# Performance work log

Hardware: AMD Instinct MI355X
Metric: run time of the kernel (lower is better)

## Reference

```python
import jax, jax.numpy as jnp
import numpy as np

B, S, D = 4, 4096, 64

def setup_inputs() -> dict:
    key = jax.random.key(0)
    kq, kk, kv = jax.random.split(key, 3)
    q = jax.random.normal(kq, (B, S, D), dtype=jnp.float32)
    k = jax.random.normal(kk, (B, S, D), dtype=jnp.float32)
    v = jax.random.normal(kv, (B, S, D), dtype=jnp.float32)
    return {"q": q, "k": k, "v": v}

def reference(q, k, v):
    d_k = k.shape[-1]
    # scores: [B, S, S]
    scores = jnp.einsum('bqd,bkd->bqk', q, k) / jnp.sqrt(jnp.asarray(d_k, q.dtype))
    s = scores.shape[-1]
    # causal mask: disallow j > i (strict upper triangle)
    causal = jnp.tril(jnp.ones((scores.shape[-2], s), dtype=bool))
    scores = jnp.where(causal, scores, jnp.asarray(-jnp.inf, scores.dtype))
    norm_scores = jax.nn.softmax(scores, axis=-1)
    return jnp.einsum('bqk,bkd->bqd', norm_scores, v)
```

## Files before the change

kernel.cpp:

```cpp
#include <hip/hip_runtime.h>

#define B_ 4
#define S_ 4096
#define D_ 64

typedef __attribute__((ext_vector_type(8))) short short8;
typedef __attribute__((ext_vector_type(4))) float f32x4;
typedef __attribute__((ext_vector_type(16))) float f32x16;
typedef __attribute__((ext_vector_type(4))) int int4v;
typedef __attribute__((ext_vector_type(2))) unsigned uint2v;
typedef unsigned short u16;

__device__ __forceinline__ unsigned pack_bf2(float a, float b) {
  unsigned ua = __float_as_uint(a) + 0x8000u;
  unsigned ub = __float_as_uint(b) + 0x8000u;
  return __builtin_amdgcn_perm(ub, ua, 0x07060302);
}

__device__ __forceinline__ float fexp2(float x) {
#if __has_builtin(__builtin_amdgcn_exp2f)
  return __builtin_amdgcn_exp2f(x);
#else
  return exp2f(x);
#endif
}

__device__ __forceinline__ uint2v permswap(unsigned a, unsigned b) {
#if __has_builtin(__builtin_amdgcn_permlane32_swap)
  return __builtin_amdgcn_permlane32_swap(a, b, false, false);
#else
  int h = (threadIdx.x >> 5) & 1;
  unsigned ta = __shfl_xor(a, 32);
  unsigned tb = __shfl_xor(b, 32);
  uint2v r;
  r[0] = h ? tb : a;
  r[1] = h ? b : ta;
  return r;
#endif
}

__global__ __launch_bounds__(256) void cvt_all_k(const float* __restrict__ q,
                                                 const float* __restrict__ k,
                                                 const float* __restrict__ v,
                                                 u16* __restrict__ wsQ,
                                                 u16* __restrict__ wsK,
                                                 u16* __restrict__ wsV) {
  int blk = blockIdx.x;
  if (blk < 1024) {
    const float* src = (blk < 512) ? q : k;
    u16* dst = (blk < 512) ? wsQ : wsK;
    float scale = (blk < 512) ? 0.18033688011112042f : 1.0f;
    int t = ((blk & 511) << 8) + threadIdx.x;
    const f32x4* s4 = (const f32x4*)src;
    f32x4 a = s4[2 * t], b = s4[2 * t + 1];
    int4v r;
    r[0] = (int)pack_bf2(a[0] * scale, a[1] * scale);
    r[1] = (int)pack_bf2(a[2] * scale, a[3] * scale);
    r[2] = (int)pack_bf2(b[0] * scale, b[1] * scale);
    r[3] = (int)pack_bf2(b[2] * scale, b[3] * scale);
    *(int4v*)(dst + 8 * (long)t) = r;
  } else {
    int t = ((blk - 1024) << 8) + threadIdx.x;
    int lane = t & 63;
    int J  = (t >> 6) & 3;
    int dt = (t >> 8) & 1;
    int ck = (t >> 9) & 63;
    int b  = t >> 15;
    int row = ck * 64 + J * 16 + (lane >> 5) * 8;
    int col = dt * 32 + (lane & 31);
    const float* src = v + ((long)(b * S_ + row)) * D_ + col;
    float e[8];
#pragma unroll
    for (int i = 0; i < 8; i++) e[i] = src[(long)i * D_];
    int4v r;
    r[0] = (int)pack_bf2(e[0], e[1]);
    r[1] = (int)pack_bf2(e[2], e[3]);
    r[2] = (int)pack_bf2(e[4], e[5]);
    r[3] = (int)pack_bf2(e[6], e[7]);
    *(int4v*)(wsV + 8 * (long)t) = r;
  }
}

#define MFMA32(a, bb, cc) __builtin_amdgcn_mfma_f32_32x32x16_bf16((a), (bb), (cc), 0, 0, 0)

__global__ __launch_bounds__(512, 2) void attn_k(const u16* __restrict__ wsQ,
                                                 const u16* __restrict__ wsK,
                                                 const u16* __restrict__ wsV,
                                                 float* __restrict__ out) {
  int bid = blockIdx.x;
  int b   = bid & 3;
  int g   = 63 - (bid >> 2);
  int tid = threadIdx.x;
  int w = tid >> 6, lane = tid & 63, c2 = lane & 31, h = lane >> 5;
  int cmax = g;
  int q0 = g * 64;

  __shared__ float sMem[8][2176];
  __shared__ float sML[8][2][32];

  float* W = &sMem[w][0];

  short8 qf[2][4];
#pragma unroll
  for (int t = 0; t < 2; t++)
#pragma unroll
    for (int kk = 0; kk < 4; kk++)
      qf[t][kk] = *(const short8*)(wsQ + ((long)(b * S_ + q0 + 32 * t + c2)) * D_ +
                                   kk * 16 + h * 8);

  f32x16 o[2][2];
#pragma unroll
  for (int t = 0; t < 2; t++)
#pragma unroll
    for (int dt = 0; dt < 2; dt++)
#pragma unroll
      for (int r = 0; r < 16; r++) o[t][dt][r] = 0.f;
  float lp[2] = {0.f, 0.f};

  const u16* kbase = wsK + ((long)(b * S_ + c2)) * D_ + h * 8;
  const u16* vbase = wsV + ((long)(b * 64)) * 4096 + (long)lane * 8;

  for (int ck = w; ck <= cmax; ck += 8) {
    const u16* kp = kbase + (long)ck * 64 * D_;
    short8 kf[2][4];
#pragma unroll
    for (int jt = 0; jt < 2; jt++)
#pragma unroll
      for (int kk = 0; kk < 4; kk++)
        kf[jt][kk] = *(const short8*)(kp + jt * 32 * D_ + kk * 16);
    const u16* vp = vbase + (long)ck * 4096;
    short8 vf[2][4];
#pragma unroll
    for (int dt = 0; dt < 2; dt++)
#pragma unroll
      for (int J = 0; J < 4; J++)
        vf[dt][J] = *(const short8*)(vp + (dt * 4 + J) * 512);

#pragma unroll
    for (int t = 0; t < 2; t++) {
      f32x16 s[2];
#pragma unroll
      for (int r = 0; r < 16; r++) { s[0][r] = 0.f; s[1][r] = 0.f; }
#pragma unroll
      for (int kk = 0; kk < 4; kk++) {
        s[0] = MFMA32(kf[0][kk], qf[t][kk], s[0]);
        s[1] = MFMA32(kf[1][kk], qf[t][kk], s[1]);
      }

      if (ck == cmax) {
        int dq = 32 * t + c2;
#pragma unroll
        for (int r = 0; r < 16; r++) {
          int row = (r & 3) + 8 * (r >> 2) + 4 * h;
          if (row      > dq) s[0][r] = -1e30f;
          if (row + 32 > dq) s[1][r] = -1e30f;
        }
      }

      float su0 = 0.f, su1 = 0.f, su2 = 0.f, su3 = 0.f;
#pragma unroll
      for (int r = 0; r < 4; r++) {
        s[0][r]      = fexp2(s[0][r]);      su0 += s[0][r];
        s[0][r + 4]  = fexp2(s[0][r + 4]);  su1 += s[0][r + 4];
        s[0][r + 8]  = fexp2(s[0][r + 8]);  su2 += s[0][r + 8];
        s[0][r + 12] = fexp2(s[0][r + 12]); su3 += s[0][r + 12];
        s[1][r]      = fexp2(s[1][r]);      su0 += s[1][r];
        s[1][r + 4]  = fexp2(s[1][r + 4]);  su1 += s[1][r + 4];
        s[1][r + 8]  = fexp2(s[1][r + 8]);  su2 += s[1][r + 8];
        s[1][r + 12] = fexp2(s[1][r + 12]); su3 += s[1][r + 12];
      }
      lp[t] += (su0 + su1) + (su2 + su3);

      short8 p[4];
#pragma unroll
      for (int jt = 0; jt < 2; jt++) {
        unsigned Dw[8];
#pragma unroll
        for (int gg = 0; gg < 4; gg++) {
          Dw[2 * gg]     = pack_bf2(s[jt][4 * gg],     s[jt][4 * gg + 1]);
          Dw[2 * gg + 1] = pack_bf2(s[jt][4 * gg + 2], s[jt][4 * gg + 3]);
        }
#pragma unroll
        for (int e = 0; e < 2; e++) {
          uint2v r0 = permswap(Dw[4 * e],     Dw[4 * e + 2]);
          uint2v r1 = permswap(Dw[4 * e + 1], Dw[4 * e + 3]);
          int4v pw;
          pw[0] = (int)r0[0]; pw[1] = (int)r1[0];
          pw[2] = (int)r0[1]; pw[3] = (int)r1[1];
          p[2 * jt + e] = __builtin_bit_cast(short8, pw);
        }
      }

#pragma unroll
      for (int J = 0; J < 4; J++) {
        o[t][0] = MFMA32(vf[0][J], p[J], o[t][0]);
        o[t][1] = MFMA32(vf[1][J], p[J], o[t][1]);
      }
    }
  }

#pragma unroll
  for (int t = 0; t < 2; t++) {
    float lt = lp[t];
    lt += __shfl_xor(lt, 32);
    if (h == 0) sML[w][t][c2] = lt;
  }

  for (int t = 0; t < 2; t++) {
    __syncthreads();
#pragma unroll
    for (int dt = 0; dt < 2; dt++)
#pragma unroll
      for (int grp = 0; grp < 4; grp++) {
        f32x4 t4;
        t4[0] = o[t][dt][4 * grp];     t4[1] = o[t][dt][4 * grp + 1];
        t4[2] = o[t][dt][4 * grp + 2]; t4[3] = o[t][dt][4 * grp + 3];
        *(f32x4*)&W[c2 * 68 + 32 * dt + 8 * grp + 4 * h] = t4;
      }
    __syncthreads();

    int q = tid >> 4, d4 = tid & 15;
    float L = 0.f;
    f32x4 acc = {0.f, 0.f, 0.f, 0.f};
#pragma unroll
    for (int w2 = 0; w2 < 8; w2++) {
      L += sML[w2][t][q];
      f32x4 pv = *(f32x4*)&sMem[w2][q * 68 + d4 * 4];
#pragma unroll
      for (int i = 0; i < 4; i++) acc[i] += pv[i];
    }
    float inv = 1.f / L;
    f32x4 r;
#pragma unroll
    for (int i = 0; i < 4; i++) r[i] = acc[i] * inv;
    *(f32x4*)(out + ((long)(b * S_ + q0 + 32 * t + q)) * D_ + d4 * 4) = r;
  }
}

extern "C" void kernel_launch(void* const* d_in, const int* in_sizes, int n_in,
                              void* d_out, int out_size, void* d_ws, size_t ws_size,
                              hipStream_t stream) {
  const float* q = (const float*)d_in[0];
  const float* k = (const float*)d_in[1];
  const float* v = (const float*)d_in[2];
  float* out = (float*)d_out;

  u16* wsQ = (u16*)d_ws;
  u16* wsK = wsQ + (long)B_ * S_ * D_;
  u16* wsV = wsK + (long)B_ * S_ * D_;

  cvt_all_k<<<1536, 256, 0, stream>>>(q, k, v, wsQ, wsK, wsV);
  attn_k<<<256, 512, 0, stream>>>(wsQ, wsK, wsV, out);
}
```

Before: 92.17 us.

## Fuse fp32-to-bf16 conversion into attention kernel, drop separate convert pass

Removes the separate conversion kernel that wrote bf16 copies of Q, K and a pre-permuted V to workspace. The attention kernel now reads fp32 Q/K/V directly and converts to bf16 in registers, applying the softmax scale to Q on load. This saves a kernel launch and a full round trip through workspace memory. In exchange, each K/V chunk is reread as fp32 and reconverted by every query block that uses it, which doubles the load bytes and adds ALU work inside the main loop. The V loads are now strided, eight separate 4-byte reads per fragment.

```diff
diff --git a/kernel.cpp b/kernel.cpp
--- a/kernel.cpp
+++ b/kernel.cpp
@@ -39,54 +39,24 @@
 #endif
 }
 
-__global__ __launch_bounds__(256) void cvt_all_k(const float* __restrict__ q,
-                                                 const float* __restrict__ k,
-                                                 const float* __restrict__ v,
-                                                 u16* __restrict__ wsQ,
-                                                 u16* __restrict__ wsK,
-                                                 u16* __restrict__ wsV) {
-  int blk = blockIdx.x;
-  if (blk < 1024) {
-    const float* src = (blk < 512) ? q : k;
-    u16* dst = (blk < 512) ? wsQ : wsK;
-    float scale = (blk < 512) ? 0.18033688011112042f : 1.0f;
-    int t = ((blk & 511) << 8) + threadIdx.x;
-    const f32x4* s4 = (const f32x4*)src;
-    f32x4 a = s4[2 * t], b = s4[2 * t + 1];
-    int4v r;
-    r[0] = (int)pack_bf2(a[0] * scale, a[1] * scale);
-    r[1] = (int)pack_bf2(a[2] * scale, a[3] * scale);
-    r[2] = (int)pack_bf2(b[0] * scale, b[1] * scale);
-    r[3] = (int)pack_bf2(b[2] * scale, b[3] * scale);
-    *(int4v*)(dst + 8 * (long)t) = r;
-  } else {
-    int t = ((blk - 1024) << 8) + threadIdx.x;
-    int lane = t & 63;
-    int J  = (t >> 6) & 3;
-    int dt = (t >> 8) & 1;
-    int ck = (t >> 9) & 63;
-    int b  = t >> 15;
-    int row = ck * 64 + J * 16 + (lane >> 5) * 8;
-    int col = dt * 32 + (lane & 31);
-    const float* src = v + ((long)(b * S_ + row)) * D_ + col;
-    float e[8];
-#pragma unroll
-    for (int i = 0; i < 8; i++) e[i] = src[(long)i * D_];
-    int4v r;
-    r[0] = (int)pack_bf2(e[0], e[1]);
-    r[1] = (int)pack_bf2(e[2], e[3]);
-    r[2] = (int)pack_bf2(e[4], e[5]);
-    r[3] = (int)pack_bf2(e[6], e[7]);
-    *(int4v*)(wsV + 8 * (long)t) = r;
-  }
+__device__ __forceinline__ short8 cvt8(const float* p, float scale) {
+  f32x4 a = *(const f32x4*)p;
+  f32x4 b = *(const f32x4*)(p + 4);
+  int4v r;
+  r[0] = (int)pack_bf2(a[0] * scale, a[1] * scale);
+  r[1] = (int)pack_bf2(a[2] * scale, a[3] * scale);
+  r[2] = (int)pack_bf2(b[0] * scale, b[1] * scale);
+  r[3] = (int)pack_bf2(b[2] * scale, b[3] * scale);
+  return __builtin_bit_cast(short8, r);
 }
 
 #define MFMA32(a, bb, cc) __builtin_amdgcn_mfma_f32_32x32x16_bf16((a), (bb), (cc), 0, 0, 0)
 
-__global__ __launch_bounds__(512, 2) void attn_k(const u16* __restrict__ wsQ,
-                                                 const u16* __restrict__ wsK,
-                                                 const u16* __restrict__ wsV,
+__global__ __launch_bounds__(512, 2) void attn_k(const float* __restrict__ Q,
+                                                 const float* __restrict__ K,
+                                                 const float* __restrict__ V,
                                                  float* __restrict__ out) {
+  const float SC = 0.18033688011112042f;
   int bid = blockIdx.x;
   int b   = bid & 3;
   int g   = 63 - (bid >> 2);
@@ -105,8 +75,7 @@
   for (int t = 0; t < 2; t++)
 #pragma unroll
     for (int kk = 0; kk < 4; kk++)
-      qf[t][kk] = *(const short8*)(wsQ + ((long)(b * S_ + q0 + 32 * t + c2)) * D_ +
-                                   kk * 16 + h * 8);
+      qf[t][kk] = cvt8(Q + ((long)(b * S_ + q0 + 32 * t + c2)) * D_ + kk * 16 + h * 8, SC);
 
   f32x16 o[2][2];
 #pragma unroll
@@ -117,24 +86,31 @@
       for (int r = 0; r < 16; r++) o[t][dt][r] = 0.f;
   float lp[2] = {0.f, 0.f};
 
-  const u16* kbase = wsK + ((long)(b * S_ + c2)) * D_ + h * 8;
-  const u16* vbase = wsV + ((long)(b * 64)) * 4096 + (long)lane * 8;
-
   for (int ck = w; ck <= cmax; ck += 8) {
-    const u16* kp = kbase + (long)ck * 64 * D_;
     short8 kf[2][4];
 #pragma unroll
-    for (int jt = 0; jt < 2; jt++)
+    for (int jt = 0; jt < 2; jt++) {
+      const float* kp = K + ((long)(b * S_ + 64 * ck + 32 * jt + c2)) * D_ + h * 8;
 #pragma unroll
       for (int kk = 0; kk < 4; kk++)
-        kf[jt][kk] = *(const short8*)(kp + jt * 32 * D_ + kk * 16);
-    const u16* vp = vbase + (long)ck * 4096;
+        kf[jt][kk] = cvt8(kp + kk * 16, 1.0f);
+    }
     short8 vf[2][4];
 #pragma unroll
     for (int dt = 0; dt < 2; dt++)
 #pragma unroll
-      for (int J = 0; J < 4; J++)
-        vf[dt][J] = *(const short8*)(vp + (dt * 4 + J) * 512);
+      for (int J = 0; J < 4; J++) {
+        const float* vp = V + ((long)(b * S_ + 64 * ck + 16 * J + 8 * h)) * D_ + 32 * dt + c2;
+        float e[8];
+#pragma unroll
+        for (int i = 0; i < 8; i++) e[i] = vp[(long)i * D_];
+        int4v r;
+        r[0] = (int)pack_bf2(e[0], e[1]);
+        r[1] = (int)pack_bf2(e[2], e[3]);
+        r[2] = (int)pack_bf2(e[4], e[5]);
+        r[3] = (int)pack_bf2(e[6], e[7]);
+        vf[dt][J] = __builtin_bit_cast(short8, r);
+      }
 
 #pragma unroll
     for (int t = 0; t < 2; t++) {
@@ -244,11 +220,5 @@
   const float* k = (const float*)d_in[1];
   const float* v = (const float*)d_in[2];
   float* out = (float*)d_out;
-
-  u16* wsQ = (u16*)d_ws;
-  u16* wsK = wsQ + (long)B_ * S_ * D_;
-  u16* wsV = wsK + (long)B_ * S_ * D_;
-
-  cvt_all_k<<<1536, 256, 0, stream>>>(q, k, v, wsQ, wsK, wsV);
-  attn_k<<<256, 512, 0, stream>>>(wsQ, wsK, wsV, out);
-}
+  attn_k<<<256, 512, 0, stream>>>(q, k, v, out);
+}
```

Result: slower. 113.8 us (+23.4%).
